# Kernel tuning notes

Hardware: AMD Instinct MI355X
Metric: run time of the kernel (lower is better)

## Reference

```python
import jax, jax.numpy as jnp
import numpy as np

EPS_IN = 1e-5   # InstanceNorm1d eps
EPS_DM = 1e-8   # demodulation eps


def _dcoef(weight, style):
    # rsqrt(sum_i (W[o,i]*s[b,i])^2 + eps) -> [B, out]
    return jax.lax.rsqrt(jnp.einsum('oi,bi->bo', jnp.square(weight), jnp.square(style)) + EPS_DM)


def setup_inputs() -> dict:
    key = jax.random.key(0)
    ks = jax.random.split(key, 7)
    B, S, H = 8, 1024, 1024
    lim = 1.0 / np.sqrt(H)
    u = lambda k, shp: jax.random.uniform(k, shp, jnp.float32, -lim, lim)
    return {
        'x': jax.random.normal(ks[0], (B, S, H), jnp.float32),
        'q_weight': u(ks[1], (H, H)),
        'k_weight': u(ks[2], (H, H)),
        'v_weight': u(ks[3], (H, H)),
        'w_weight': u(ks[4], (H, H)),
        'u_weight': u(ks[5], (H, H)),
        'styles': jax.random.normal(ks[6], (B, 2 * H), jnp.float32) * 0.5 + 1.0,
        'num_heads': 16,
    }


def reference(x, q_weight, k_weight, v_weight, w_weight, u_weight, styles, num_heads):
    B, S, H = x.shape
    nh = num_heads
    d = H // nh
    scale = jnp.asarray(d, x.dtype) ** -0.5

    s1 = styles[:, :H]   # modulates input hidden dim of q/k/v
    s2 = styles[:, H:]   # modulates input hidden dim of w/u and v output

    # per-sample modulation + InstanceNorm over hidden dim
    x = x * s1[:, None, :]
    mu = jnp.mean(x, axis=-1, keepdims=True)
    var = jnp.mean(jnp.square(x - mu), axis=-1, keepdims=True)
    x = (x - mu) * jax.lax.rsqrt(var + EPS_IN)

    q_dc = _dcoef(q_weight, s1)  # [B,H]
    k_dc = _dcoef(k_weight, s1)
    v_dc = _dcoef(v_weight, s1)
    w_dc = _dcoef(w_weight, s2)
    u_dc = _dcoef(u_weight, s2)

    def heads(t):  # [B,S,H] -> [B,nh,S,d]
        return t.reshape(B, S, nh, d).transpose(0, 2, 1, 3)

    q = heads(jnp.einsum('bsh,oh->bso', x, q_weight) * q_dc[:, None, :])
    k = heads(jnp.einsum('bsh,oh->bso', x, k_weight) * k_dc[:, None, :])
    v_flat = jnp.einsum('bsh,oh->bso', x, v_weight) * v_dc[:, None, :] * s2[:, None, :]
    skip = v_flat
    v = heads(v_flat)

    attn = jnp.einsum('bhqd,bhkd->bhqk', q, k) * scale
    attn = jax.nn.softmax(attn, axis=-1)
    out = jnp.einsum('bhqk,bhkd->bhqd', attn, v).transpose(0, 2, 1, 3).reshape(B, S, H)

    out = jnp.einsum('bsh,oh->bso', out, w_weight) * w_dc[:, None, :]
    skip = jnp.einsum('bsh,oh->bso', skip, u_weight) * u_dc[:, None, :]
    return out + skip
```

## Files before the change

kernel.cpp:

```cpp
#include <hip/hip_runtime.h>
#include <hip/hip_bf16.h>

#define B_ 8
#define S_ 1024
#define H_ 1024
#define NH 16
#define DH 64
#define BS (B_*S_)
#define L2E 1.44269504f

typedef unsigned short u16;
typedef __attribute__((ext_vector_type(8))) short bf16x8;
typedef __attribute__((ext_vector_type(4))) float f32x4;
typedef __attribute__((ext_vector_type(16))) float f32x16;
typedef __attribute__((ext_vector_type(4))) u16 u16x4;
typedef __attribute__((ext_vector_type(2))) unsigned int u32x2;

#define MFMA(a,b,c)   __builtin_amdgcn_mfma_f32_16x16x32_bf16((a),(b),(c),0,0,0)
#define MFMA32(a,b,c) __builtin_amdgcn_mfma_f32_32x32x16_bf16((a),(b),(c),0,0,0)

__device__ __forceinline__ u16 f2bf(float f) {
  union { float f; unsigned u; } v; v.f = f;
  unsigned r = v.u + 0x7fffu + ((v.u >> 16) & 1u);
  return (u16)(r >> 16);
}

__device__ __forceinline__ unsigned packbf2(float a, float b) {
  union { __hip_bfloat162 h; unsigned u; } v;
  v.h = __float22bfloat162_rn(float2{a, b});
  return v.u;
}

__device__ __forceinline__ void gload16(const u16* g, u16* l) {
  __builtin_amdgcn_global_load_lds(
      (const __attribute__((address_space(1))) unsigned int*)g,
      (__attribute__((address_space(3))) unsigned int*)l, 16, 0, 0);
}

__global__ __launch_bounds__(256) void dcoef_kernel(
    const float* __restrict__ qw, const float* __restrict__ kw,
    const float* __restrict__ vw, const float* __restrict__ ww,
    const float* __restrict__ uw, const float* __restrict__ styles,
    float* __restrict__ dc, u16* __restrict__ w16) {
  int bi = blockIdx.x;
  int wsel = bi >> 10;
  int o = bi & 1023;
  const float* W = (wsel == 0) ? qw : (wsel == 1) ? kw : (wsel == 2) ? vw
                   : (wsel == 3) ? ww : uw;
  int soff = (wsel < 3) ? 0 : H_;
  int tid = threadIdx.x;
  float4 w4 = *(const float4*)(W + (size_t)o * H_ + tid * 4);
  u16x4 wo = { f2bf(w4.x), f2bf(w4.y), f2bf(w4.z), f2bf(w4.w) };
  *(u16x4*)(w16 + (size_t)wsel * H_ * H_ + (size_t)o * H_ + tid * 4) = wo;
  float w2x = w4.x * w4.x, w2y = w4.y * w4.y, w2z = w4.z * w4.z, w2w = w4.w * w4.w;
  float acc[8];
#pragma unroll
  for (int b = 0; b < 8; b++) {
    float4 s4 = *(const float4*)(styles + (size_t)b * 2 * H_ + soff + tid * 4);
    acc[b] = w2x * s4.x * s4.x + w2y * s4.y * s4.y + w2z * s4.z * s4.z + w2w * s4.w * s4.w;
  }
#pragma unroll
  for (int off = 1; off < 64; off <<= 1)
#pragma unroll
    for (int b = 0; b < 8; b++) acc[b] += __shfl_xor(acc[b], off);
  __shared__ float red[4][8];
  int w = tid >> 6, l = tid & 63;
  if (l == 0)
#pragma unroll
    for (int b = 0; b < 8; b++) red[w][b] = acc[b];
  __syncthreads();
  if (tid < 8) {
    int b = tid;
    float v = red[0][b] + red[1][b] + red[2][b] + red[3][b];
    float r = rsqrtf(v + 1e-8f);
    if (wsel == 2) r *= styles[(size_t)b * 2 * H_ + H_ + o];
    dc[(size_t)wsel * B_ * H_ + b * H_ + o] = r;
  }
}

__global__ __launch_bounds__(256) void ln_kernel(
    const float* __restrict__ x, const float* __restrict__ styles,
    u16* __restrict__ xn) {
  int row = blockIdx.x;
  int b = row >> 10;
  int tid = threadIdx.x;
  const float4 xv = *(const float4*)(x + (size_t)row * H_ + tid * 4);
  const float4 sv = *(const float4*)(styles + (size_t)b * 2 * H_ + tid * 4);
  float v0 = xv.x * sv.x, v1 = xv.y * sv.y, v2 = xv.z * sv.z, v3 = xv.w * sv.w;
  float sum = v0 + v1 + v2 + v3;
  float sq = v0 * v0 + v1 * v1 + v2 * v2 + v3 * v3;
#pragma unroll
  for (int off = 1; off < 64; off <<= 1) {
    sum += __shfl_xor(sum, off);
    sq += __shfl_xor(sq, off);
  }
  __shared__ float rsum[4], rsq[4];
  int w = tid >> 6;
  if ((tid & 63) == 0) { rsum[w] = sum; rsq[w] = sq; }
  __syncthreads();
  sum = rsum[0] + rsum[1] + rsum[2] + rsum[3];
  sq = rsq[0] + rsq[1] + rsq[2] + rsq[3];
  float mean = sum * (1.f / H_);
  float var = sq * (1.f / H_) - mean * mean;
  float rstd = rsqrtf(var + 1e-5f);
  u16x4 o = { f2bf((v0 - mean) * rstd), f2bf((v1 - mean) * rstd),
              f2bf((v2 - mean) * rstd), f2bf((v3 - mean) * rstd) };
  *(u16x4*)(xn + (size_t)row * H_ + tid * 4) = o;
}

__device__ __forceinline__ void gemm128_core(
    const u16* __restrict__ Arow, const u16* __restrict__ Brow, int K,
    u16* ldsA, u16* ldsB, f32x4 acc[4][4]) {
  const int tid = threadIdx.x;
  const int l = tid & 63, w = tid >> 6;
  const int wm = (w >> 1) * 64, wn = (w & 1) * 64;
  const int lrow = l & 15, lko = (l >> 4) * 8;
  const int srow = tid >> 2;
  const int scol = (tid & 3) * 8;
  for (int k0 = 0; k0 < K; k0 += 32) {
    __syncthreads();
    gload16(Arow + (size_t)srow * K + k0 + scol,        ldsA + srow * 32 + scol);
    gload16(Arow + (size_t)(srow + 64) * K + k0 + scol, ldsA + (srow + 64) * 32 + scol);
    gload16(Brow + (size_t)srow * K + k0 + scol,        ldsB + srow * 32 + scol);
    gload16(Brow + (size_t)(srow + 64) * K + k0 + scol, ldsB + (srow + 64) * 32 + scol);
    __syncthreads();
    bf16x8 af[4], bfr[4];
#pragma unroll
    for (int i = 0; i < 4; i++)
      af[i] = *(const bf16x8*)&ldsA[(wm + i * 16 + lrow) * 32 + lko];
#pragma unroll
    for (int i = 0; i < 4; i++)
      bfr[i] = *(const bf16x8*)&ldsB[(wn + i * 16 + lrow) * 32 + lko];
#pragma unroll
    for (int mi = 0; mi < 4; mi++)
#pragma unroll
      for (int ni = 0; ni < 4; ni++)
        acc[mi][ni] = MFMA(af[mi], bfr[ni], acc[mi][ni]);
  }
}

__global__ __launch_bounds__(256) void qkv_kernel(
    const u16* __restrict__ xn, const u16* __restrict__ w16,
    const float* __restrict__ dc, u16* __restrict__ Qb, u16* __restrict__ Kb,
    u16* __restrict__ VT, u16* __restrict__ vfl) {
  __shared__ u16 ldsA[128 * 32], ldsB[128 * 32];
  int bm = blockIdx.x;
  int bn = blockIdx.y;
  f32x4 acc[4][4] = {};
  gemm128_core(xn + (size_t)bm * 128 * H_, w16 + (size_t)bn * 128 * H_, H_,
               ldsA, ldsB, acc);
  int l = threadIdx.x & 63, w = threadIdx.x >> 6;
  int wm = (w >> 1) * 64, wn = (w & 1) * 64;
  int wsel = bn >> 3;
  int col0 = (bn & 7) * 128 + wn;
  int row0 = bm * 128 + wm;
  const float* dcw = dc + (size_t)wsel * B_ * H_;
  float extra = (wsel == 0) ? 0.125f * L2E : 1.0f;
#pragma unroll
  for (int mi = 0; mi < 4; mi++) {
#pragma unroll
    for (int ni = 0; ni < 4; ni++) {
      int col = col0 + ni * 16 + (l & 15);
      int hh = col >> 6, dd = col & 63;
      int s_base = (row0 + mi * 16 + (l >> 4) * 4) & 1023;
      int b = (row0 + mi * 16 + (l >> 4) * 4) >> 10;
      float dcv = dcw[b * H_ + col] * extra;
      u16 bv[4];
#pragma unroll
      for (int rr = 0; rr < 4; rr++)
        bv[rr] = f2bf(acc[mi][ni][rr] * dcv);
      if (wsel == 0) {
#pragma unroll
        for (int rr = 0; rr < 4; rr++)
          Qb[((size_t)(b * NH + hh) * S_ + s_base + rr) * DH + dd] = bv[rr];
      } else if (wsel == 1) {
#pragma unroll
        for (int rr = 0; rr < 4; rr++)
          Kb[((size_t)(b * NH + hh) * S_ + s_base + rr) * DH + dd] = bv[rr];
      } else {
        u16x4 pv = { bv[0], bv[1], bv[2], bv[3] };
        *(u16x4*)&VT[((size_t)(b * NH + hh) * DH + dd) * S_ + s_base] = pv;
#pragma unroll
        for (int rr = 0; rr < 4; rr++)
          vfl[(size_t)(row0 + mi * 16 + (l >> 4) * 4 + rr) * H_ + col] = bv[rr];
      }
    }
  }
}

__global__ __launch_bounds__(512) void attn_kernel(
    const u16* __restrict__ Qb, const u16* __restrict__ Kb,
    const u16* __restrict__ VT, u16* __restrict__ xat) {
  __shared__ u16 ldsK[3][64 * 64];
  __shared__ u16 ldsV[3][64 * 64];
  int tid = threadIdx.x;
  int l = tid & 63, w = tid >> 6;
  int id = blockIdx.x;
  int r = id & 7, rest = id >> 3;
  int qblk = rest & 3, a = rest >> 2;
  int hl = a * 8 + r;
  int h = hl & 15, b = hl >> 4;
  int q0 = qblk * 256 + w * 32;
  const u16* Qp = Qb + ((size_t)(b * NH + h) * S_ + q0) * DH;
  const u16* Kp = Kb + (size_t)(b * NH + h) * S_ * DH;
  const u16* Vp = VT + (size_t)(b * NH + h) * DH * S_;
  int lq = l & 31, hi = l >> 5;
  int srow = tid >> 3, schunk = tid & 7;
  int ssw = (schunk * 8) ^ ((srow & 7) << 3);
  const u16* Ksrc = Kp + (size_t)srow * DH + ssw;
  const u16* Vsrc = Vp + (size_t)srow * S_ + ssw;
  int sdst = srow * 64 + schunk * 8;
  gload16(Ksrc, &ldsK[0][sdst]);
  gload16(Vsrc, &ldsV[0][sdst]);
  gload16(Ksrc + 64 * DH, &ldsK[1][sdst]);
  gload16(Vsrc + 64,      &ldsV[1][sdst]);
  bf16x8 qf[4];
#pragma unroll
  for (int s = 0; s < 4; s++)
    qf[s] = *(const bf16x8*)(Qp + lq * 64 + s * 16 + hi * 8);
  f32x16 acc0 = {}, acc1 = {};
  float ls = 0.f;
  asm volatile("s_waitcnt vmcnt(2)" ::: "memory");
  __builtin_amdgcn_s_barrier();
  int cur = 0;
  for (int t = 0; t < 16; ++t) {
    if (t + 2 < 16) {
      int nb = cur + 2; if (nb >= 3) nb -= 3;
      gload16(Ksrc + (size_t)(t + 2) * 64 * DH, &ldsK[nb][sdst]);
      gload16(Vsrc + (size_t)(t + 2) * 64,      &ldsV[nb][sdst]);
    }
    const u16* Kt = &ldsK[cur][0];
    const u16* Vt = &ldsV[cur][0];
    f32x16 z0 = {}, z1 = {};
    __builtin_amdgcn_s_setprio(1);
#pragma unroll
    for (int s = 0; s < 4; s++) {
      int ch = ((s * 2 + hi) ^ (lq & 7)) * 8;
      bf16x8 kf0 = *(const bf16x8*)&Kt[lq * 64 + ch];
      bf16x8 kf1 = *(const bf16x8*)&Kt[(32 + lq) * 64 + ch];
      z0 = MFMA32(kf0, qf[s], z0);
      z1 = MFMA32(kf1, qf[s], z1);
    }
    __builtin_amdgcn_s_setprio(0);
    float rs = 0.f;
#pragma unroll
    for (int i = 0; i < 16; i++) {
      z0[i] = __builtin_exp2f(z0[i]); rs += z0[i];
      z1[i] = __builtin_exp2f(z1[i]); rs += z1[i];
    }
    rs += __shfl_xor(rs, 32);
    ls += rs;
    bf16x8 pf[4];
#pragma unroll
    for (int g = 0; g < 2; g++) {
      unsigned pa = packbf2(z0[g * 8 + 0], z0[g * 8 + 1]);
      unsigned pb = packbf2(z0[g * 8 + 2], z0[g * 8 + 3]);
      unsigned pc = packbf2(z0[g * 8 + 4], z0[g * 8 + 5]);
      unsigned pd = packbf2(z0[g * 8 + 6], z0[g * 8 + 7]);
      u32x2 sA = __builtin_amdgcn_permlane32_swap(pa, pc, false, false);
      u32x2 sB = __builtin_amdgcn_permlane32_swap(pb, pd, false, false);
      union { unsigned u[4]; bf16x8 v; } uu;
      uu.u[0] = sA[0]; uu.u[1] = sB[0]; uu.u[2] = sA[1]; uu.u[3] = sB[1];
      pf[g] = uu.v;
    }
#pragma unroll
    for (int g = 0; g < 2; g++) {
      unsigned pa = packbf2(z1[g * 8 + 0], z1[g * 8 + 1]);
      unsigned pb = packbf2(z1[g * 8 + 2], z1[g * 8 + 3]);
      unsigned pc = packbf2(z1[g * 8 + 4], z1[g * 8 + 5]);
      unsigned pd = packbf2(z1[g * 8 + 6], z1[g * 8 + 7]);
      u32x2 sA = __builtin_amdgcn_permlane32_swap(pa, pc, false, false);
      u32x2 sB = __builtin_amdgcn_permlane32_swap(pb, pd, false, false);
      union { unsigned u[4]; bf16x8 v; } uu;
      uu.u[0] = sA[0]; uu.u[1] = sB[0]; uu.u[2] = sA[1]; uu.u[3] = sB[1];
      pf[2 + g] = uu.v;
    }
    __builtin_amdgcn_s_setprio(1);
#pragma unroll
    for (int ks = 0; ks < 4; ks++) {
      int ch = ((ks * 2 + hi) ^ (lq & 7)) * 8;
      bf16x8 vf0 = *(const bf16x8*)&Vt[lq * 64 + ch];
      bf16x8 vf1 = *(const bf16x8*)&Vt[(32 + lq) * 64 + ch];
      acc0 = MFMA32(vf0, pf[ks], acc0);
      acc1 = MFMA32(vf1, pf[ks], acc1);
    }
    __builtin_amdgcn_s_setprio(0);
    if (t < 14) {
      asm volatile("s_waitcnt vmcnt(2)" ::: "memory");
    } else if (t == 14) {
      asm volatile("s_waitcnt vmcnt(0)" ::: "memory");
    }
    if (t < 15) __builtin_amdgcn_s_barrier();
    cur = (cur == 2) ? 0 : cur + 1;
  }
  float inv = 1.f / ls;
  size_t orow = ((size_t)b * S_ + q0 + lq) * H_ + h * DH;
#pragma unroll
  for (int g = 0; g < 4; g++) {
    int d0 = g * 8 + hi * 4;
    u16x4 o0 = { f2bf(acc0[g * 4 + 0] * inv), f2bf(acc0[g * 4 + 1] * inv),
                 f2bf(acc0[g * 4 + 2] * inv), f2bf(acc0[g * 4 + 3] * inv) };
    *(u16x4*)(xat + orow + d0) = o0;
    u16x4 o1 = { f2bf(acc1[g * 4 + 0] * inv), f2bf(acc1[g * 4 + 1] * inv),
                 f2bf(acc1[g * 4 + 2] * inv), f2bf(acc1[g * 4 + 3] * inv) };
    *(u16x4*)(xat + orow + 32 + d0) = o1;
  }
}

__global__ __launch_bounds__(256) void out_kernel(
    const u16* __restrict__ xat, const u16* __restrict__ vfl,
    const u16* __restrict__ w16, const float* __restrict__ dc,
    float* __restrict__ out) {
  __shared__ u16 ldsA[128 * 32], ldsB[128 * 32];
  int bm = blockIdx.x;
  int bn = blockIdx.y;
  f32x4 acc[4][4] = {};
  gemm128_core(xat + (size_t)bm * 128 * H_,
               w16 + (size_t)3 * H_ * H_ + (size_t)bn * 128 * H_, H_,
               ldsA, ldsB, acc);
  int l = threadIdx.x & 63, w = threadIdx.x >> 6;
  int wm = (w >> 1) * 64, wn = (w & 1) * 64;
  int col0 = bn * 128 + wn;
  int row0 = bm * 128 + wm;
  int b = row0 >> 10;
  const float* wdc = dc + (size_t)3 * B_ * H_ + b * H_;
  const float* udc = dc + (size_t)4 * B_ * H_ + b * H_;
  float ratio[4], ud[4];
#pragma unroll
  for (int ni = 0; ni < 4; ni++) {
    int col = col0 + ni * 16 + (l & 15);
    ud[ni] = udc[col];
    ratio[ni] = wdc[col] / ud[ni];
  }
#pragma unroll
  for (int mi = 0; mi < 4; mi++)
#pragma unroll
    for (int ni = 0; ni < 4; ni++)
#pragma unroll
      for (int rr = 0; rr < 4; rr++) acc[mi][ni][rr] *= ratio[ni];
  gemm128_core(vfl + (size_t)bm * 128 * H_,
               w16 + (size_t)4 * H_ * H_ + (size_t)bn * 128 * H_, H_,
               ldsA, ldsB, acc);
#pragma unroll
  for (int mi = 0; mi < 4; mi++)
#pragma unroll
    for (int ni = 0; ni < 4; ni++) {
      int col = col0 + ni * 16 + (l & 15);
#pragma unroll
      for (int rr = 0; rr < 4; rr++) {
        int row = row0 + mi * 16 + (l >> 4) * 4 + rr;
        out[(size_t)row * H_ + col] = acc[mi][ni][rr] * ud[ni];
      }
    }
}

extern "C" void kernel_launch(void* const* d_in, const int* in_sizes, int n_in,
                              void* d_out, int out_size, void* d_ws, size_t ws_size,
                              hipStream_t stream) {
  const float* x = (const float*)d_in[0];
  const float* qw = (const float*)d_in[1];
  const float* kw = (const float*)d_in[2];
  const float* vw = (const float*)d_in[3];
  const float* ww = (const float*)d_in[4];
  const float* uw = (const float*)d_in[5];
  const float* styles = (const float*)d_in[6];
  float* out = (float*)d_out;

  char* ws = (char*)d_ws;
  size_t need = 163840 + (size_t)5 * H_ * H_ * 2 + (size_t)6 * BS * H_ * 2;
  if (ws_size < need) return;
  float* dc = (float*)ws;
  u16* w16 = (u16*)(ws + 163840);
  u16* xn  = w16 + (size_t)5 * H_ * H_;
  u16* Qb  = xn + (size_t)BS * H_;
  u16* Kb  = Qb + (size_t)BS * H_;
  u16* VT  = Kb + (size_t)BS * H_;
  u16* vfl = VT + (size_t)BS * H_;
  u16* xat = vfl + (size_t)BS * H_;

  dcoef_kernel<<<dim3(5 * H_), dim3(256), 0, stream>>>(qw, kw, vw, ww, uw, styles, dc, w16);
  ln_kernel<<<dim3(BS), dim3(256), 0, stream>>>(x, styles, xn);
  qkv_kernel<<<dim3(64, 24), dim3(256), 0, stream>>>(xn, w16, dc, Qb, Kb, VT, vfl);
  attn_kernel<<<dim3(512), dim3(512), 0, stream>>>(Qb, Kb, VT, xat);
  out_kernel<<<dim3(64, 8), dim3(256), 0, stream>>>(xat, vfl, w16, dc, out);
}
```

Baseline: 201.8 us.

## Rewrite QKV GEMM as 256x256 tile, double-buffered, swizzled LDS pipeline

```diff
diff --git a/kernel.cpp b/kernel.cpp
--- a/kernel.cpp
+++ b/kernel.cpp
@@ -108,6 +108,194 @@
   *(u16x4*)(xn + (size_t)row * H_ + tid * 4) = o;
 }
 
+__global__ __launch_bounds__(512) void qkv_kernel(
+    const u16* __restrict__ xn, const u16* __restrict__ w16,
+    const float* __restrict__ dc, u16* __restrict__ Qb, u16* __restrict__ Kb,
+    u16* __restrict__ VT, u16* __restrict__ vfl) {
+  __shared__ u16 lA[2][2][128 * 64];
+  __shared__ u16 lB[2][2][128 * 64];
+  int bid = blockIdx.x;
+  int swz = (bid & 7) * 48 + (bid >> 3);
+  int bm = swz / 12, bn = swz % 12;
+  const u16* A  = xn + (size_t)bm * 256 * H_;
+  const u16* Bp = w16 + (size_t)bn * 256 * H_;
+  int tid = threadIdx.x;
+  int l = tid & 63, wid = tid >> 6;
+  int wr = wid >> 2, wc = wid & 3;
+  int lrow = l & 15, kc = l >> 4;
+  int sch = tid & 7, sr0 = tid >> 3;
+  int slch = sch ^ (sr0 & 7);
+  const size_t sSrc = (size_t)sr0 * H_ + slch * 8;
+  const int sDst = sr0 * 64 + sch * 8;
+#define STG(srcbase, dstarr) do { \
+    gload16((srcbase) + sSrc, (dstarr) + sDst); \
+    gload16((srcbase) + sSrc + (size_t)64 * H_, (dstarr) + sDst + 64 * 64); } while (0)
+  const int chk0 = ((kc) ^ (lrow & 7)) * 8;
+  const int chk1 = ((4 + kc) ^ (lrow & 7)) * 8;
+  const u16* Ah0 = lA[0][wr];
+  const u16* Ah1 = lA[1][wr];
+  const u16* Bh0 = lB[0][wc >> 1];
+  const u16* Bh1 = lB[1][wc >> 1];
+  const int brow = (wc & 1) * 64;
+  STG(Bp,                         lB[0][0]);
+  STG(Bp + (size_t)128 * H_,      lB[0][1]);
+  STG(A,                          lA[0][0]);
+  STG(A + (size_t)128 * H_,       lA[0][1]);
+  STG(Bp + 64,                    lB[1][0]);
+  STG(Bp + (size_t)128 * H_ + 64, lB[1][1]);
+  STG(A + 64,                     lA[1][0]);
+  STG(A + (size_t)128 * H_ + 64,  lA[1][1]);
+  asm volatile("s_waitcnt vmcnt(8)" ::: "memory");
+  __builtin_amdgcn_s_barrier();
+  f32x4 acc[8][4] = {};
+  bf16x8 af[4][2], bfA[2][2], bfB[2][2];
+#define PH_SYNC \
+    __builtin_amdgcn_s_barrier(); \
+    asm volatile("s_waitcnt lgkmcnt(0)" ::: "memory"); \
+    __builtin_amdgcn_sched_barrier(0)
+#define QMFMA(MO, NO, BF) \
+    __builtin_amdgcn_s_setprio(1); \
+    _Pragma("unroll") \
+    for (int mi = 0; mi < 4; mi++) \
+      _Pragma("unroll") \
+      for (int ni = 0; ni < 2; ni++) { \
+        acc[MO + mi][NO + ni] = MFMA(af[mi][0], BF[ni][0], acc[MO + mi][NO + ni]); \
+        acc[MO + mi][NO + ni] = MFMA(af[mi][1], BF[ni][1], acc[MO + mi][NO + ni]); \
+      } \
+    __builtin_amdgcn_s_setprio(0)
+  for (int i = 0; i < 8; ++i) {
+    const int k2 = (2 * i + 2) * 64;
+    const int k3 = (2 * i + 3) * 64;
+    const bool more = (i < 7);
+#pragma unroll
+    for (int mi = 0; mi < 4; mi++) {
+      af[mi][0] = *(const bf16x8*)&Ah0[(mi * 16 + lrow) * 64 + chk0];
+      af[mi][1] = *(const bf16x8*)&Ah0[(mi * 16 + lrow) * 64 + chk1];
+    }
+#pragma unroll
+    for (int ni = 0; ni < 2; ni++) {
+      bfA[ni][0] = *(const bf16x8*)&Bh0[(brow + ni * 16 + lrow) * 64 + chk0];
+      bfA[ni][1] = *(const bf16x8*)&Bh0[(brow + ni * 16 + lrow) * 64 + chk1];
+    }
+    PH_SYNC;
+    QMFMA(0, 0, bfA);
+    __builtin_amdgcn_s_barrier();
+#pragma unroll
+    for (int ni = 0; ni < 2; ni++) {
+      bfB[ni][0] = *(const bf16x8*)&Bh0[(brow + (2 + ni) * 16 + lrow) * 64 + chk0];
+      bfB[ni][1] = *(const bf16x8*)&Bh0[(brow + (2 + ni) * 16 + lrow) * 64 + chk1];
+    }
+    PH_SYNC;
+    QMFMA(0, 2, bfB);
+    __builtin_amdgcn_s_barrier();
+#pragma unroll
+    for (int mi = 0; mi < 4; mi++) {
+      af[mi][0] = *(const bf16x8*)&Ah0[((64 + mi * 16) + lrow) * 64 + chk0];
+      af[mi][1] = *(const bf16x8*)&Ah0[((64 + mi * 16) + lrow) * 64 + chk1];
+    }
+    if (more) {
+      STG(Bp + k2,                    lB[0][0]);
+      STG(Bp + (size_t)128 * H_ + k2, lB[0][1]);
+    }
+    PH_SYNC;
+    QMFMA(4, 0, bfA);
+    __builtin_amdgcn_s_barrier();
+    if (more) {
+      STG(A + k2,                    lA[0][0]);
+      STG(A + (size_t)128 * H_ + k2, lA[0][1]);
+    }
+    __builtin_amdgcn_s_barrier();
+    QMFMA(4, 2, bfB);
+    if (more) {
+      asm volatile("s_waitcnt vmcnt(8)" ::: "memory");
+    } else {
+      asm volatile("s_waitcnt vmcnt(0)" ::: "memory");
+    }
+    __builtin_amdgcn_s_barrier();
+#pragma unroll
+    for (int mi = 0; mi < 4; mi++) {
+      af[mi][0] = *(const bf16x8*)&Ah1[(mi * 16 + lrow) * 64 + chk0];
+      af[mi][1] = *(const bf16x8*)&Ah1[(mi * 16 + lrow) * 64 + chk1];
+    }
+#pragma unroll
+    for (int ni = 0; ni < 2; ni++) {
+      bfA[ni][0] = *(const bf16x8*)&Bh1[(brow + ni * 16 + lrow) * 64 + chk0];
+      bfA[ni][1] = *(const bf16x8*)&Bh1[(brow + ni * 16 + lrow) * 64 + chk1];
+    }
+    PH_SYNC;
+    QMFMA(0, 0, bfA);
+    __builtin_amdgcn_s_barrier();
+#pragma unroll
+    for (int ni = 0; ni < 2; ni++) {
+      bfB[ni][0] = *(const bf16x8*)&Bh1[(brow + (2 + ni) * 16 + lrow) * 64 + chk0];
+      bfB[ni][1] = *(const bf16x8*)&Bh1[(brow + (2 + ni) * 16 + lrow) * 64 + chk1];
+    }
+    PH_SYNC;
+    QMFMA(0, 2, bfB);
+    __builtin_amdgcn_s_barrier();
+#pragma unroll
+    for (int mi = 0; mi < 4; mi++) {
+      af[mi][0] = *(const bf16x8*)&Ah1[((64 + mi * 16) + lrow) * 64 + chk0];
+      af[mi][1] = *(const bf16x8*)&Ah1[((64 + mi * 16) + lrow) * 64 + chk1];
+    }
+    if (more) {
+      STG(Bp + k3,                    lB[1][0]);
+      STG(Bp + (size_t)128 * H_ + k3, lB[1][1]);
+    }
+    PH_SYNC;
+    QMFMA(4, 0, bfA);
+    __builtin_amdgcn_s_barrier();
+    if (more) {
+      STG(A + k3,                    lA[1][0]);
+      STG(A + (size_t)128 * H_ + k3, lA[1][1]);
+    }
+    __builtin_amdgcn_s_barrier();
+    QMFMA(4, 2, bfB);
+    if (more) {
+      asm volatile("s_waitcnt vmcnt(8)" ::: "memory");
+    }
+    __builtin_amdgcn_s_barrier();
+  }
+#undef STG
+#undef PH_SYNC
+#undef QMFMA
+  int wsel = bn >> 2;
+  int colm = (bn & 3) * 256 + wc * 64;
+  int row0 = bm * 256 + wr * 128;
+  const float* dcw = dc + (size_t)wsel * B_ * H_;
+  float extra = (wsel == 0) ? 0.125f * L2E : 1.0f;
+#pragma unroll
+  for (int mi = 0; mi < 8; mi++) {
+    int row = row0 + mi * 16 + (l >> 4) * 4;
+    int b = row >> 10, s_base = row & 1023;
+#pragma unroll
+    for (int ni = 0; ni < 4; ni++) {
+      int col = colm + ni * 16 + lrow;
+      int hh = col >> 6, dd = col & 63;
+      float dcv = dcw[b * H_ + col] * extra;
+      u16 bv[4];
+#pragma unroll
+      for (int rr = 0; rr < 4; rr++)
+        bv[rr] = f2bf(acc[mi][ni][rr] * dcv);
+      if (wsel == 0) {
+#pragma unroll
+        for (int rr = 0; rr < 4; rr++)
+          Qb[((size_t)(b * NH + hh) * S_ + s_base + rr) * DH + dd] = bv[rr];
+      } else if (wsel == 1) {
+#pragma unroll
+        for (int rr = 0; rr < 4; rr++)
+          Kb[((size_t)(b * NH + hh) * S_ + s_base + rr) * DH + dd] = bv[rr];
+      } else {
+        u16x4 pv = { bv[0], bv[1], bv[2], bv[3] };
+        *(u16x4*)&VT[((size_t)(b * NH + hh) * DH + dd) * S_ + s_base] = pv;
+#pragma unroll
+        for (int rr = 0; rr < 4; rr++)
+          vfl[(size_t)(row + rr) * H_ + col] = bv[rr];
+      }
+    }
+  }
+}
+
 __device__ __forceinline__ void gemm128_core(
     const u16* __restrict__ Arow, const u16* __restrict__ Brow, int K,
     u16* ldsA, u16* ldsB, f32x4 acc[4][4]) {
@@ -136,55 +324,6 @@
 #pragma unroll
       for (int ni = 0; ni < 4; ni++)
         acc[mi][ni] = MFMA(af[mi], bfr[ni], acc[mi][ni]);
-  }
-}
-
-__global__ __launch_bounds__(256) void qkv_kernel(
-    const u16* __restrict__ xn, const u16* __restrict__ w16,
-    const float* __restrict__ dc, u16* __restrict__ Qb, u16* __restrict__ Kb,
-    u16* __restrict__ VT, u16* __restrict__ vfl) {
-  __shared__ u16 ldsA[128 * 32], ldsB[128 * 32];
-  int bm = blockIdx.x;
-  int bn = blockIdx.y;
-  f32x4 acc[4][4] = {};
-  gemm128_core(xn + (size_t)bm * 128 * H_, w16 + (size_t)bn * 128 * H_, H_,
-               ldsA, ldsB, acc);
-  int l = threadIdx.x & 63, w = threadIdx.x >> 6;
-  int wm = (w >> 1) * 64, wn = (w & 1) * 64;
-  int wsel = bn >> 3;
-  int col0 = (bn & 7) * 128 + wn;
-  int row0 = bm * 128 + wm;
-  const float* dcw = dc + (size_t)wsel * B_ * H_;
-  float extra = (wsel == 0) ? 0.125f * L2E : 1.0f;
-#pragma unroll
-  for (int mi = 0; mi < 4; mi++) {
-#pragma unroll
-    for (int ni = 0; ni < 4; ni++) {
-      int col = col0 + ni * 16 + (l & 15);
-      int hh = col >> 6, dd = col & 63;
-      int s_base = (row0 + mi * 16 + (l >> 4) * 4) & 1023;
-      int b = (row0 + mi * 16 + (l >> 4) * 4) >> 10;
-      float dcv = dcw[b * H_ + col] * extra;
-      u16 bv[4];
-#pragma unroll
-      for (int rr = 0; rr < 4; rr++)
-        bv[rr] = f2bf(acc[mi][ni][rr] * dcv);
-      if (wsel == 0) {
-#pragma unroll
-        for (int rr = 0; rr < 4; rr++)
-          Qb[((size_t)(b * NH + hh) * S_ + s_base + rr) * DH + dd] = bv[rr];
-      } else if (wsel == 1) {
-#pragma unroll
-        for (int rr = 0; rr < 4; rr++)
-          Kb[((size_t)(b * NH + hh) * S_ + s_base + rr) * DH + dd] = bv[rr];
-      } else {
-        u16x4 pv = { bv[0], bv[1], bv[2], bv[3] };
-        *(u16x4*)&VT[((size_t)(b * NH + hh) * DH + dd) * S_ + s_base] = pv;
-#pragma unroll
-        for (int rr = 0; rr < 4; rr++)
-          vfl[(size_t)(row0 + mi * 16 + (l >> 4) * 4 + rr) * H_ + col] = bv[rr];
-      }
-    }
   }
 }
 
@@ -380,7 +519,7 @@
 
   dcoef_kernel<<<dim3(5 * H_), dim3(256), 0, stream>>>(qw, kw, vw, ww, uw, styles, dc, w16);
   ln_kernel<<<dim3(BS), dim3(256), 0, stream>>>(x, styles, xn);
-  qkv_kernel<<<dim3(64, 24), dim3(256), 0, stream>>>(xn, w16, dc, Qb, Kb, VT, vfl);
+  qkv_kernel<<<dim3(384), dim3(512), 0, stream>>>(xn, w16, dc, Qb, Kb, VT, vfl);
   attn_kernel<<<dim3(512), dim3(512), 0, stream>>>(Qb, Kb, VT, xat);
   out_kernel<<<dim3(64, 8), dim3(256), 0, stream>>>(xat, vfl, w16, dc, out);
 }
```

New measurement: 204.8 us. Within noise of the previous version (+1.5%).

## Interleave the two output GEMMs in one K-loop with separate accumulators

Applied to the files above, without the earlier changes.

```diff
diff --git a/kernel.cpp b/kernel.cpp
--- a/kernel.cpp
+++ b/kernel.cpp
@@ -311,36 +311,60 @@
     const u16* __restrict__ xat, const u16* __restrict__ vfl,
     const u16* __restrict__ w16, const float* __restrict__ dc,
     float* __restrict__ out) {
-  __shared__ u16 ldsA[128 * 32], ldsB[128 * 32];
+  __shared__ u16 ldsA1[128 * 32], ldsB1[128 * 32];
+  __shared__ u16 ldsA2[128 * 32], ldsB2[128 * 32];
   int bm = blockIdx.x;
   int bn = blockIdx.y;
-  f32x4 acc[4][4] = {};
-  gemm128_core(xat + (size_t)bm * 128 * H_,
-               w16 + (size_t)3 * H_ * H_ + (size_t)bn * 128 * H_, H_,
-               ldsA, ldsB, acc);
-  int l = threadIdx.x & 63, w = threadIdx.x >> 6;
-  int wm = (w >> 1) * 64, wn = (w & 1) * 64;
+  const u16* A1 = xat + (size_t)bm * 128 * H_;
+  const u16* A2 = vfl + (size_t)bm * 128 * H_;
+  const u16* B1 = w16 + (size_t)3 * H_ * H_ + (size_t)bn * 128 * H_;
+  const u16* B2 = w16 + (size_t)4 * H_ * H_ + (size_t)bn * 128 * H_;
+  const int tid = threadIdx.x;
+  const int l = tid & 63, w = tid >> 6;
+  const int wm = (w >> 1) * 64, wn = (w & 1) * 64;
+  const int lrow = l & 15, lko = (l >> 4) * 8;
+  const int srow = tid >> 2;
+  const int scol = (tid & 3) * 8;
+  f32x4 accW[4][4] = {}, accU[4][4] = {};
+  for (int k0 = 0; k0 < H_; k0 += 32) {
+    __syncthreads();
+    gload16(A1 + (size_t)srow * H_ + k0 + scol,        ldsA1 + srow * 32 + scol);
+    gload16(A1 + (size_t)(srow + 64) * H_ + k0 + scol, ldsA1 + (srow + 64) * 32 + scol);
+    gload16(B1 + (size_t)srow * H_ + k0 + scol,        ldsB1 + srow * 32 + scol);
+    gload16(B1 + (size_t)(srow + 64) * H_ + k0 + scol, ldsB1 + (srow + 64) * 32 + scol);
+    gload16(A2 + (size_t)srow * H_ + k0 + scol,        ldsA2 + srow * 32 + scol);
+    gload16(A2 + (size_t)(srow + 64) * H_ + k0 + scol, ldsA2 + (srow + 64) * 32 + scol);
+    gload16(B2 + (size_t)srow * H_ + k0 + scol,        ldsB2 + srow * 32 + scol);
+    gload16(B2 + (size_t)(srow + 64) * H_ + k0 + scol, ldsB2 + (srow + 64) * 32 + scol);
+    __syncthreads();
+    bf16x8 af1[4], bf1[4], af2[4], bf2[4];
+#pragma unroll
+    for (int i = 0; i < 4; i++) {
+      af1[i] = *(const bf16x8*)&ldsA1[(wm + i * 16 + lrow) * 32 + lko];
+      bf1[i] = *(const bf16x8*)&ldsB1[(wn + i * 16 + lrow) * 32 + lko];
+      af2[i] = *(const bf16x8*)&ldsA2[(wm + i * 16 + lrow) * 32 + lko];
+      bf2[i] = *(const bf16x8*)&ldsB2[(wn + i * 16 + lrow) * 32 + lko];
+    }
+#pragma unroll
+    for (int mi = 0; mi < 4; mi++)
+#pragma unroll
+      for (int ni = 0; ni < 4; ni++) {
+        accW[mi][ni] = MFMA(af1[mi], bf1[ni], accW[mi][ni]);
+        accU[mi][ni] = MFMA(af2[mi], bf2[ni], accU[mi][ni]);
+      }
+  }
   int col0 = bn * 128 + wn;
   int row0 = bm * 128 + wm;
   int b = row0 >> 10;
   const float* wdc = dc + (size_t)3 * B_ * H_ + b * H_;
   const float* udc = dc + (size_t)4 * B_ * H_ + b * H_;
-  float ratio[4], ud[4];
+  float wd[4], ud[4];
 #pragma unroll
   for (int ni = 0; ni < 4; ni++) {
     int col = col0 + ni * 16 + (l & 15);
+    wd[ni] = wdc[col];
     ud[ni] = udc[col];
-    ratio[ni] = wdc[col] / ud[ni];
-  }
-#pragma unroll
-  for (int mi = 0; mi < 4; mi++)
-#pragma unroll
-    for (int ni = 0; ni < 4; ni++)
-#pragma unroll
-      for (int rr = 0; rr < 4; rr++) acc[mi][ni][rr] *= ratio[ni];
-  gemm128_core(vfl + (size_t)bm * 128 * H_,
-               w16 + (size_t)4 * H_ * H_ + (size_t)bn * 128 * H_, H_,
-               ldsA, ldsB, acc);
+  }
 #pragma unroll
   for (int mi = 0; mi < 4; mi++)
 #pragma unroll
@@ -349,7 +373,8 @@
 #pragma unroll
       for (int rr = 0; rr < 4; rr++) {
         int row = row0 + mi * 16 + (l >> 4) * 4 + rr;
-        out[(size_t)row * H_ + col] = acc[mi][ni][rr] * ud[ni];
+        out[(size_t)row * H_ + col] =
+            accW[mi][ni][rr] * wd[ni] + accU[mi][ni][rr] * ud[ni];
       }
     }
 }
```

After: 230.3 us. 1.14x slower.
